# Performance work log

Hardware: AMD Instinct MI355X
Metric: run time of the kernel (lower is better)

Reference implementation:

```python
import jax, jax.numpy as jnp
import numpy as np

VOCAB = 32000
EMBED = 512
HIDDEN = 1024
ATT_L = 64
MAX_LEN = 32
BATCH = 64  # hardcoded in original get_start_states()


def setup_inputs() -> dict:
    key = jax.random.key(0)
    ks = jax.random.split(key, 12)
    s = 0.02
    return {
        "features": jax.random.normal(ks[0], (BATCH, ATT_L, HIDDEN), dtype=jnp.float32),
        "captions": jax.random.randint(ks[1], (BATCH, MAX_LEN), 0, VOCAB),
        "lengths": jnp.full((BATCH,), MAX_LEN - 1, dtype=jnp.int32),  # full lengths (sorted)
        "embed_table": jax.random.normal(ks[2], (VOCAB, EMBED), dtype=jnp.float32) * s,
        "W_ih": jax.random.normal(ks[3], (4 * HIDDEN, EMBED + HIDDEN), dtype=jnp.float32) * s,
        "W_hh": jax.random.normal(ks[4], (4 * HIDDEN, HIDDEN), dtype=jnp.float32) * s,
        "b_ih": jax.random.normal(ks[5], (4 * HIDDEN,), dtype=jnp.float32) * s,
        "b_hh": jax.random.normal(ks[6], (4 * HIDDEN,), dtype=jnp.float32) * s,
        "attn_W": jax.random.normal(ks[7], (ATT_L, EMBED + HIDDEN), dtype=jnp.float32) * s,
        "attn_b": jax.random.normal(ks[8], (ATT_L,), dtype=jnp.float32) * s,
        "lin_W": jax.random.normal(ks[9], (VOCAB, HIDDEN), dtype=jnp.float32) * s,
        "lin_b": jax.random.normal(ks[10], (VOCAB,), dtype=jnp.float32) * s,
    }


def reference(features, captions, lengths, embed_table, W_ih, W_hh, b_ih, b_hh,
              attn_W, attn_b, lin_W, lin_b):
    B = features.shape[0]
    T = captions.shape[1] - 1  # loop runs max_seq_length - 1 steps
    emb = embed_table[captions]              # (B, S, E)
    xs = jnp.transpose(emb[:, :T, :], (1, 0, 2))  # (T, B, E) time-major for scan

    h0 = jnp.zeros((B, HIDDEN), dtype=features.dtype)
    c0 = jnp.zeros((B, HIDDEN), dtype=features.dtype)

    def step(carry, x_t):
        h, c = carry
        # additive-attention branch (softmax over a singleton dim, as in original)
        att_cat = jnp.concatenate([x_t, h], axis=-1) @ attn_W.T + attn_b  # (B, L)
        att_w = jax.nn.softmax(jax.nn.relu(att_cat)[:, None, :], axis=1)  # (B, 1, L) -> all ones
        ctx = jnp.einsum('bol,blh->bh', att_w, features)                  # (B, H)
        # LSTM step (PyTorch gate order: i, f, g, o)
        lstm_in = jnp.concatenate([x_t, ctx], axis=-1)  # (B, E+H)
        gates = lstm_in @ W_ih.T + b_ih + h @ W_hh.T + b_hh
        i, f, g, o = jnp.split(gates, 4, axis=-1)
        c_new = jax.nn.sigmoid(f) * c + jax.nn.sigmoid(i) * jnp.tanh(g)
        h_new = jax.nn.sigmoid(o) * jnp.tanh(c_new)
        return (h_new, c_new), h_new

    _, hs = jax.lax.scan(step, (h0, c0), xs)  # (T, B, H)
    logits = hs @ lin_W.T + lin_b             # (T, B, V)
    # pack_padded_sequence with full lengths == time-major flatten
    return logits.reshape(T * B, -1)
```

## Files before the change

kernel.cpp:

```cpp
#include <hip/hip_runtime.h>
#include <hip/hip_bf16.h>
#include <stdint.h>

#define T_STEPS 31
#define B_ 64
#define E_ 512
#define H_ 1024
#define G4 4096
#define V_ 32000
#define MPAD 2048

typedef __bf16 bf16x8_t __attribute__((ext_vector_type(8)));
typedef float f32x4_t __attribute__((ext_vector_type(4)));
typedef unsigned short u16x8_t __attribute__((ext_vector_type(8)));
using bf16 = __hip_bfloat16;

typedef const __attribute__((address_space(1))) unsigned int gas_u32;
typedef __attribute__((address_space(3))) unsigned int las_u32;

__device__ __forceinline__ void async16(const bf16* g, bf16* l) {
    __builtin_amdgcn_global_load_lds((gas_u32*)(uintptr_t)g, (las_u32*)(uintptr_t)l, 16, 0, 0);
}

template<int BM, int BN>
__global__ __launch_bounds__(256)
void gemm_lds(const bf16* __restrict__ A, const bf16* __restrict__ BT,
              float* __restrict__ C, const float* __restrict__ bias,
              int M, int N, int K, int accumulate)
{
    constexpr int BK = 32;
    constexpr int WM = BM / 2, WN = BN / 2;
    constexpr int MI = WM / 16, NI = WN / 16;
    constexpr int AV = (BM * BK) / (8 * 256);
    constexpr int BV = (BN * BK) / (8 * 256);
    static_assert(AV >= 1 && BV >= 1, "tile too small for staging");

    __shared__ bf16 As[BM * BK];
    __shared__ bf16 Bs[BN * BK];

    const int tid = threadIdx.x;
    const int lane = tid & 63;
    const int w = tid >> 6;
    const int wr = w >> 1, wc = w & 1;
    const int quad = lane >> 4, l16 = lane & 15;
    const int m0 = blockIdx.x * BM;
    const int n0 = blockIdx.y * BN;

    f32x4_t acc[MI][NI];
#pragma unroll
    for (int i = 0; i < MI; i++)
#pragma unroll
        for (int j = 0; j < NI; j++) acc[i][j] = f32x4_t{0.f, 0.f, 0.f, 0.f};

    for (int kt = 0; kt < K; kt += BK) {
#pragma unroll
        for (int v = 0; v < AV; v++) {
            int idx = tid + v * 256;
            int row = idx >> 2, col = (idx & 3) << 3;
            async16(A + (size_t)(m0 + row) * K + kt + col, As + idx * 8);
        }
#pragma unroll
        for (int v = 0; v < BV; v++) {
            int idx = tid + v * 256;
            int row = idx >> 2, col = (idx & 3) << 3;
            async16(BT + (size_t)(n0 + row) * K + kt + col, Bs + idx * 8);
        }
        __syncthreads();

        bf16x8_t af[MI], bfr[NI];
#pragma unroll
        for (int i = 0; i < MI; i++)
            af[i] = __builtin_bit_cast(bf16x8_t,
                *reinterpret_cast<const u16x8_t*>(&As[(wr * WM + i * 16 + l16) * BK + quad * 8]));
#pragma unroll
        for (int j = 0; j < NI; j++)
            bfr[j] = __builtin_bit_cast(bf16x8_t,
                *reinterpret_cast<const u16x8_t*>(&Bs[(wc * WN + j * 16 + l16) * BK + quad * 8]));
#pragma unroll
        for (int i = 0; i < MI; i++)
#pragma unroll
            for (int j = 0; j < NI; j++)
                acc[i][j] = __builtin_amdgcn_mfma_f32_16x16x32_bf16(af[i], bfr[j], acc[i][j], 0, 0, 0);
        __syncthreads();
    }

#pragma unroll
    for (int i = 0; i < MI; i++) {
        int rbase = m0 + wr * WM + i * 16 + quad * 4;
#pragma unroll
        for (int j = 0; j < NI; j++) {
            int coln = n0 + wc * WN + j * 16 + l16;
            float badd = bias ? bias[coln] : 0.f;
#pragma unroll
            for (int r = 0; r < 4; r++) {
                int grow = rbase + r;
                if (grow < M) {
                    size_t ci = (size_t)grow * N + coln;
                    float val = acc[i][j][r] + badd;
                    if (accumulate) C[ci] += val; else C[ci] = val;
                }
            }
        }
    }
}

__global__ __launch_bounds__(256)
void step_fused(const bf16* __restrict__ h_in, const bf16* __restrict__ Whh,
                const float* __restrict__ pre_x, const float* __restrict__ ctxW,
                const float* __restrict__ bc, float* __restrict__ c,
                bf16* __restrict__ h_out, bf16* __restrict__ hs, int t)
{
    constexpr int BK = 32;
    constexpr int K = H_;
    __shared__ bf16 As[64 * BK];
    __shared__ bf16 Bs[64 * BK];
    __shared__ float gates[64 * 65];

    const int tid = threadIdx.x;
    const int lane = tid & 63;
    const int w = tid >> 6;
    const int wr = w >> 1, wc = w & 1;
    const int quad = lane >> 4, l16 = lane & 15;
    const int n0 = blockIdx.x * 64;

    f32x4_t acc[2][2];
#pragma unroll
    for (int i = 0; i < 2; i++)
#pragma unroll
        for (int j = 0; j < 2; j++) acc[i][j] = f32x4_t{0.f, 0.f, 0.f, 0.f};

    for (int kt = 0; kt < K; kt += BK) {
        {
            int row = tid >> 2, col = (tid & 3) << 3;
            async16(h_in + (size_t)row * K + kt + col, As + tid * 8);
            async16(Whh + (size_t)(n0 + row) * K + kt + col, Bs + tid * 8);
        }
        __syncthreads();
        bf16x8_t af[2], bfr[2];
#pragma unroll
        for (int i = 0; i < 2; i++)
            af[i] = __builtin_bit_cast(bf16x8_t,
                *reinterpret_cast<const u16x8_t*>(&As[(wr * 32 + i * 16 + l16) * BK + quad * 8]));
#pragma unroll
        for (int j = 0; j < 2; j++)
            bfr[j] = __builtin_bit_cast(bf16x8_t,
                *reinterpret_cast<const u16x8_t*>(&Bs[(wc * 32 + j * 16 + l16) * BK + quad * 8]));
#pragma unroll
        for (int i = 0; i < 2; i++)
#pragma unroll
            for (int j = 0; j < 2; j++)
                acc[i][j] = __builtin_amdgcn_mfma_f32_16x16x32_bf16(af[i], bfr[j], acc[i][j], 0, 0, 0);
        __syncthreads();
    }

#pragma unroll
    for (int i = 0; i < 2; i++) {
        int rbase = wr * 32 + i * 16 + quad * 4;
#pragma unroll
        for (int j = 0; j < 2; j++) {
            int col = wc * 32 + j * 16 + l16;
            int gcol = n0 + col;
            float badd = bc[gcol];
#pragma unroll
            for (int r = 0; r < 4; r++) {
                int b = rbase + r;
                gates[b * 65 + col] = acc[i][j][r] + badd
                    + pre_x[((size_t)t * B_ + b) * G4 + gcol]
                    + ctxW[(size_t)b * G4 + gcol];
            }
        }
    }
    __syncthreads();

#pragma unroll
    for (int v = 0; v < 4; v++) {
        int item = tid + v * 256;
        int b = item >> 4, jj = item & 15;
        float gi = gates[b * 65 + jj * 4 + 0];
        float gf = gates[b * 65 + jj * 4 + 1];
        float gg = gates[b * 65 + jj * 4 + 2];
        float go = gates[b * 65 + jj * 4 + 3];
        int j = (n0 >> 2) + jj;
        int idx = b * H_ + j;
        float si = 1.f / (1.f + expf(-gi));
        float sf = 1.f / (1.f + expf(-gf));
        float so = 1.f / (1.f + expf(-go));
        float cn = sf * c[idx] + si * tanhf(gg);
        float hn = so * tanhf(cn);
        c[idx] = cn;
        bf16 hb = __float2bfloat16(hn);
        h_out[idx] = hb;
        hs[((size_t)t * B_ + b) * H_ + j] = hb;
    }
}


__global__ void ctx_kernel(const float* __restrict__ features, bf16* __restrict__ hi, bf16* __restrict__ lo)
{
    int b = blockIdx.x;
    for (int j = threadIdx.x; j < H_; j += 256) {
        float s = 0.f;
        const float* f = features + (size_t)b * 64 * H_ + j;
#pragma unroll
        for (int l = 0; l < 64; l++) s += f[(size_t)l * H_];
        bf16 h = __float2bfloat16(s);
        hi[b * H_ + j] = h;
        lo[b * H_ + j] = __float2bfloat16(s - __bfloat162float(h));
    }
}

__global__ void bias_kernel(const float* __restrict__ bi, const float* __restrict__ bh, float* __restrict__ bc)
{
    int g = blockIdx.x * 256 + threadIdx.x;
    if (g < G4) bc[(g & (H_ - 1)) * 4 + (g >> 10)] = bi[g] + bh[g];
}

__global__ void gather_embed(const int* __restrict__ captions, const float* __restrict__ table,
                             bf16* __restrict__ xs)
{
    int idx = blockIdx.x * 256 + threadIdx.x;
    int tb = idx >> 9, e = idx & (E_ - 1);
    float v = 0.f;
    if (tb < T_STEPS * B_) {
        int t = tb >> 6, b = tb & 63;
        int tok = captions[b * 32 + t];
        v = table[(size_t)tok * E_ + e];
    }
    xs[idx] = __float2bfloat16(v);
}

__global__ void cvt_bf16(const float* __restrict__ src, bf16* __restrict__ hi, bf16* __restrict__ lo,
                         int rows, int cols, int stride, int off, int perm)
{
    long i4 = (long)blockIdx.x * 256 + threadIdx.x;
    long total = (long)rows * cols / 4;
    if (i4 >= total) return;
    long e = i4 * 4;
    int r = (int)(e / cols);
    int ci = (int)(e % cols);
    int ro = perm ? ((r & (H_ - 1)) * 4 + (r >> 10)) : r;
    f32x4_t v = *reinterpret_cast<const f32x4_t*>(src + (size_t)r * stride + off + ci);
    size_t ob = (size_t)ro * cols + ci;
#pragma unroll
    for (int q = 0; q < 4; q++) {
        bf16 h = __float2bfloat16(v[q]);
        hi[ob + q] = h;
        if (lo) lo[ob + q] = __float2bfloat16(v[q] - __bfloat162float(h));
    }
}

__global__ void zero_f32(float* __restrict__ p, int n)
{
    int i = blockIdx.x * 256 + threadIdx.x;
    if (i < n) p[i] = 0.f;
}
__global__ void zero_bf16(bf16* __restrict__ p, int n)
{
    int i = blockIdx.x * 256 + threadIdx.x;
    if (i < n) p[i] = __float2bfloat16(0.f);
}

extern "C" void kernel_launch(void* const* d_in, const int* in_sizes, int n_in,
                              void* d_out, int out_size, void* d_ws, size_t ws_size,
                              hipStream_t stream)
{
    (void)in_sizes; (void)n_in; (void)out_size; (void)ws_size;
    const float* features = (const float*)d_in[0];
    const int*   captions = (const int*)d_in[1];
    const float* embed    = (const float*)d_in[3];
    const float* W_ih     = (const float*)d_in[4];
    const float* W_hh     = (const float*)d_in[5];
    const float* b_ih     = (const float*)d_in[6];
    const float* b_hh     = (const float*)d_in[7];
    const float* lin_W    = (const float*)d_in[10];
    const float* lin_b    = (const float*)d_in[11];
    float* out = (float*)d_out;

    char* wp = (char*)d_ws;
    auto alloc = [&](size_t bytes) -> void* {
        void* p = (void*)wp;
        wp += (bytes + 255) & ~(size_t)255;
        return p;
    };
    bf16*  ctx_hi = (bf16*)alloc((size_t)B_ * H_ * 2);
    bf16*  ctx_lo = (bf16*)alloc((size_t)B_ * H_ * 2);
    float* bc     = (float*)alloc((size_t)G4 * 4);
    bf16*  xs     = (bf16*)alloc((size_t)MPAD * E_ * 2);
    bf16*  Wx     = (bf16*)alloc((size_t)G4 * E_ * 2);
    bf16*  Wc_hi  = (bf16*)alloc((size_t)G4 * H_ * 2);
    bf16*  Wc_lo  = (bf16*)alloc((size_t)G4 * H_ * 2);
    bf16*  Whh    = (bf16*)alloc((size_t)G4 * H_ * 2);
    bf16*  WlinB  = (bf16*)alloc((size_t)V_ * H_ * 2);
    float* pre_x  = (float*)alloc((size_t)T_STEPS * B_ * G4 * 4);
    float* ctxW   = (float*)alloc((size_t)B_ * G4 * 4);
    float* cbuf   = (float*)alloc((size_t)B_ * H_ * 4);
    bf16*  h_bf   = (bf16*)alloc((size_t)B_ * H_ * 2);
    bf16*  hs     = (bf16*)alloc((size_t)MPAD * H_ * 2);

    bias_kernel<<<16, 256, 0, stream>>>(b_ih, b_hh, bc);
    ctx_kernel<<<B_, 256, 0, stream>>>(features, ctx_hi, ctx_lo);
    gather_embed<<<MPAD * E_ / 256, 256, 0, stream>>>(captions, embed, xs);
    cvt_bf16<<<G4 * E_ / 4 / 256, 256, 0, stream>>>(W_ih, Wx, nullptr, G4, E_, E_ + H_, 0, 1);
    cvt_bf16<<<G4 * H_ / 4 / 256, 256, 0, stream>>>(W_ih, Wc_hi, Wc_lo, G4, H_, E_ + H_, E_, 1);
    cvt_bf16<<<G4 * H_ / 4 / 256, 256, 0, stream>>>(W_hh, Whh, nullptr, G4, H_, H_, 0, 1);
    cvt_bf16<<<V_ * (H_ / 4) / 256, 256, 0, stream>>>(lin_W, WlinB, nullptr, V_, H_, H_, 0, 0);
    zero_f32<<<B_ * H_ / 256, 256, 0, stream>>>(cbuf, B_ * H_);
    zero_bf16<<<B_ * H_ / 256, 256, 0, stream>>>(h_bf, B_ * H_);
    zero_bf16<<<(MPAD - T_STEPS * B_) * H_ / 256, 256, 0, stream>>>(
        hs + (size_t)T_STEPS * B_ * H_, (MPAD - T_STEPS * B_) * H_);

    gemm_lds<64, 64><<<dim3(1, G4 / 64), 256, 0, stream>>>(ctx_hi, Wc_hi, ctxW, nullptr, B_, G4, H_, 0);
    gemm_lds<64, 64><<<dim3(1, G4 / 64), 256, 0, stream>>>(ctx_lo, Wc_hi, ctxW, nullptr, B_, G4, H_, 1);
    gemm_lds<64, 64><<<dim3(1, G4 / 64), 256, 0, stream>>>(ctx_hi, Wc_lo, ctxW, nullptr, B_, G4, H_, 1);

    gemm_lds<128, 128><<<dim3(MPAD / 128, G4 / 128), 256, 0, stream>>>(
        xs, Wx, pre_x, nullptr, T_STEPS * B_, G4, E_, 0);

    for (int t = 0; t < T_STEPS; t++)
        step_fused<<<G4 / 64, 256, 0, stream>>>(h_bf, Whh, pre_x, ctxW, bc, cbuf, h_bf, hs, t);

    gemm_lds<128, 128><<<dim3(MPAD / 128, V_ / 128), 256, 0, stream>>>(
        hs, WlinB, out, lin_b, T_STEPS * B_, V_, H_, 0);
}
```

Baseline: 1.220 ms.

## Replace per-step LSTM launches with persistent recurrence kernel and XCD-aware GEMM tiling

The 31 per-timestep launches become one persistent kernel of 64 workgroups. Each workgroup keeps its 64-row slice of W_hh resident in swizzled LDS (128 KB) and the cell state in registers, and uses an atomic grid barrier between steps. This removes per-step launch overhead and the repeated reloading of W_hh from global memory. Separately, the GEMMs now use a 1D grid remapped so that neighbouring tiles land on the same XCD for better L2 reuse. The risks are that the spin barrier can deadlock if all 64 blocks are not co-resident, and that h is read directly from global memory on each step.

```diff
diff --git a/kernel.cpp b/kernel.cpp
--- a/kernel.cpp
+++ b/kernel.cpp
@@ -9,6 +9,7 @@
 #define G4 4096
 #define V_ 32000
 #define MPAD 2048
+#define NREC 64
 
 typedef __bf16 bf16x8_t __attribute__((ext_vector_type(8)));
 typedef float f32x4_t __attribute__((ext_vector_type(4)));
@@ -26,7 +27,7 @@
 __global__ __launch_bounds__(256)
 void gemm_lds(const bf16* __restrict__ A, const bf16* __restrict__ BT,
               float* __restrict__ C, const float* __restrict__ bias,
-              int M, int N, int K, int accumulate)
+              int M, int N, int K, int accumulate, int mblocks)
 {
     constexpr int BK = 32;
     constexpr int WM = BM / 2, WN = BN / 2;
@@ -43,8 +44,14 @@
     const int w = tid >> 6;
     const int wr = w >> 1, wc = w & 1;
     const int quad = lane >> 4, l16 = lane & 15;
-    const int m0 = blockIdx.x * BM;
-    const int n0 = blockIdx.y * BN;
+
+    const int nwg = gridDim.x;
+    const int bid = blockIdx.x;
+    const int q = nwg >> 3, r = nwg & 7;
+    const int xcd = bid & 7, o = bid >> 3;
+    const int wgid = (xcd < r ? xcd * (q + 1) : r * (q + 1) + (xcd - r) * q) + o;
+    const int m0 = (wgid % mblocks) * BM;
+    const int n0 = (wgid / mblocks) * BN;
 
     f32x4_t acc[MI][NI];
 #pragma unroll
@@ -104,16 +111,25 @@
     }
 }
 
+__device__ __forceinline__ void grid_barrier(int* bar, int target) {
+    __syncthreads();
+    if (threadIdx.x == 0) {
+        __threadfence();
+        atomicAdd(bar, 1);
+        while (__hip_atomic_load(bar, __ATOMIC_ACQUIRE, __HIP_MEMORY_SCOPE_AGENT) < target)
+            __builtin_amdgcn_s_sleep(2);
+        __threadfence();
+    }
+    __syncthreads();
+}
+
 __global__ __launch_bounds__(256)
-void step_fused(const bf16* __restrict__ h_in, const bf16* __restrict__ Whh,
-                const float* __restrict__ pre_x, const float* __restrict__ ctxW,
-                const float* __restrict__ bc, float* __restrict__ c,
-                bf16* __restrict__ h_out, bf16* __restrict__ hs, int t)
-{
-    constexpr int BK = 32;
-    constexpr int K = H_;
-    __shared__ bf16 As[64 * BK];
-    __shared__ bf16 Bs[64 * BK];
+void recurrence(const bf16* __restrict__ h0, bf16* __restrict__ hs,
+                const bf16* __restrict__ Whh, const float* __restrict__ pre_x,
+                const float* __restrict__ ctxW, const float* __restrict__ bc,
+                int* __restrict__ bar)
+{
+    __shared__ bf16 Wl[64 * H_];
     __shared__ float gates[64 * 65];
 
     const int tid = threadIdx.x;
@@ -123,74 +139,87 @@
     const int quad = lane >> 4, l16 = lane & 15;
     const int n0 = blockIdx.x * 64;
 
-    f32x4_t acc[2][2];
-#pragma unroll
-    for (int i = 0; i < 2; i++)
-#pragma unroll
-        for (int j = 0; j < 2; j++) acc[i][j] = f32x4_t{0.f, 0.f, 0.f, 0.f};
-
-    for (int kt = 0; kt < K; kt += BK) {
-        {
-            int row = tid >> 2, col = (tid & 3) << 3;
-            async16(h_in + (size_t)row * K + kt + col, As + tid * 8);
-            async16(Whh + (size_t)(n0 + row) * K + kt + col, Bs + tid * 8);
+#pragma unroll 4
+    for (int ck = tid; ck < 64 * 128; ck += 256) {
+        int row = ck >> 7, c16 = ck & 127;
+        u16x8_t v = *reinterpret_cast<const u16x8_t*>(Whh + (size_t)(n0 + row) * H_ + (c16 << 3));
+        int byte = (row << 11) + (((c16 << 4)) ^ ((row & 7) << 4));
+        *reinterpret_cast<u16x8_t*>(reinterpret_cast<char*>(Wl) + byte) = v;
+    }
+
+    float creg[4] = {0.f, 0.f, 0.f, 0.f};
+    __syncthreads();
+
+    const int arow = wr * 32 + l16;
+    const int r0 = wc * 32 + l16;
+    const int xr = (r0 & 7) << 4;
+    const char* wl0 = reinterpret_cast<const char*>(Wl) + (r0 << 11);
+    const char* wl1 = reinterpret_cast<const char*>(Wl) + ((r0 + 16) << 11);
+
+    int target = NREC;
+    for (int t = 0; t < T_STEPS; t++) {
+        const bf16* hp = t ? hs + (size_t)(t - 1) * B_ * H_ : h0;
+        const bf16* ha0 = hp + (size_t)arow * H_ + quad * 8;
+        const bf16* ha1 = ha0 + 16 * H_;
+
+        f32x4_t acc[2][2];
+#pragma unroll
+        for (int i = 0; i < 2; i++)
+#pragma unroll
+            for (int j = 0; j < 2; j++) acc[i][j] = f32x4_t{0.f, 0.f, 0.f, 0.f};
+
+#pragma unroll 4
+        for (int kt = 0; kt < H_; kt += 32) {
+            int off = ((kt << 1) + (quad << 4)) ^ xr;
+            bf16x8_t a0 = __builtin_bit_cast(bf16x8_t, *reinterpret_cast<const u16x8_t*>(ha0 + kt));
+            bf16x8_t a1 = __builtin_bit_cast(bf16x8_t, *reinterpret_cast<const u16x8_t*>(ha1 + kt));
+            bf16x8_t b0 = __builtin_bit_cast(bf16x8_t, *reinterpret_cast<const u16x8_t*>(wl0 + off));
+            bf16x8_t b1 = __builtin_bit_cast(bf16x8_t, *reinterpret_cast<const u16x8_t*>(wl1 + off));
+            acc[0][0] = __builtin_amdgcn_mfma_f32_16x16x32_bf16(a0, b0, acc[0][0], 0, 0, 0);
+            acc[0][1] = __builtin_amdgcn_mfma_f32_16x16x32_bf16(a0, b1, acc[0][1], 0, 0, 0);
+            acc[1][0] = __builtin_amdgcn_mfma_f32_16x16x32_bf16(a1, b0, acc[1][0], 0, 0, 0);
+            acc[1][1] = __builtin_amdgcn_mfma_f32_16x16x32_bf16(a1, b1, acc[1][1], 0, 0, 0);
+        }
+
+#pragma unroll
+        for (int i = 0; i < 2; i++) {
+            int rbase = wr * 32 + i * 16 + quad * 4;
+#pragma unroll
+            for (int j = 0; j < 2; j++) {
+                int col = wc * 32 + j * 16 + l16;
+                int gcol = n0 + col;
+                float badd = bc[gcol];
+#pragma unroll
+                for (int r = 0; r < 4; r++) {
+                    int b = rbase + r;
+                    gates[b * 65 + col] = acc[i][j][r] + badd
+                        + pre_x[((size_t)t * B_ + b) * G4 + gcol]
+                        + ctxW[(size_t)b * G4 + gcol];
+                }
+            }
         }
         __syncthreads();
-        bf16x8_t af[2], bfr[2];
-#pragma unroll
-        for (int i = 0; i < 2; i++)
-            af[i] = __builtin_bit_cast(bf16x8_t,
-                *reinterpret_cast<const u16x8_t*>(&As[(wr * 32 + i * 16 + l16) * BK + quad * 8]));
-#pragma unroll
-        for (int j = 0; j < 2; j++)
-            bfr[j] = __builtin_bit_cast(bf16x8_t,
-                *reinterpret_cast<const u16x8_t*>(&Bs[(wc * 32 + j * 16 + l16) * BK + quad * 8]));
-#pragma unroll
-        for (int i = 0; i < 2; i++)
-#pragma unroll
-            for (int j = 0; j < 2; j++)
-                acc[i][j] = __builtin_amdgcn_mfma_f32_16x16x32_bf16(af[i], bfr[j], acc[i][j], 0, 0, 0);
-        __syncthreads();
-    }
-
-#pragma unroll
-    for (int i = 0; i < 2; i++) {
-        int rbase = wr * 32 + i * 16 + quad * 4;
-#pragma unroll
-        for (int j = 0; j < 2; j++) {
-            int col = wc * 32 + j * 16 + l16;
-            int gcol = n0 + col;
-            float badd = bc[gcol];
-#pragma unroll
-            for (int r = 0; r < 4; r++) {
-                int b = rbase + r;
-                gates[b * 65 + col] = acc[i][j][r] + badd
-                    + pre_x[((size_t)t * B_ + b) * G4 + gcol]
-                    + ctxW[(size_t)b * G4 + gcol];
-            }
-        }
-    }
-    __syncthreads();
-
-#pragma unroll
-    for (int v = 0; v < 4; v++) {
-        int item = tid + v * 256;
-        int b = item >> 4, jj = item & 15;
-        float gi = gates[b * 65 + jj * 4 + 0];
-        float gf = gates[b * 65 + jj * 4 + 1];
-        float gg = gates[b * 65 + jj * 4 + 2];
-        float go = gates[b * 65 + jj * 4 + 3];
-        int j = (n0 >> 2) + jj;
-        int idx = b * H_ + j;
-        float si = 1.f / (1.f + expf(-gi));
-        float sf = 1.f / (1.f + expf(-gf));
-        float so = 1.f / (1.f + expf(-go));
-        float cn = sf * c[idx] + si * tanhf(gg);
-        float hn = so * tanhf(cn);
-        c[idx] = cn;
-        bf16 hb = __float2bfloat16(hn);
-        h_out[idx] = hb;
-        hs[((size_t)t * B_ + b) * H_ + j] = hb;
+
+#pragma unroll
+        for (int v = 0; v < 4; v++) {
+            int item = tid + v * 256;
+            int b = item >> 4, jj = item & 15;
+            float gi = gates[b * 65 + jj * 4 + 0];
+            float gf = gates[b * 65 + jj * 4 + 1];
+            float gg = gates[b * 65 + jj * 4 + 2];
+            float go = gates[b * 65 + jj * 4 + 3];
+            int j = (n0 >> 2) + jj;
+            float si = 1.f / (1.f + expf(-gi));
+            float sf = 1.f / (1.f + expf(-gf));
+            float so = 1.f / (1.f + expf(-go));
+            float cn = sf * creg[v] + si * tanhf(gg);
+            float hn = so * tanhf(cn);
+            creg[v] = cn;
+            hs[((size_t)t * B_ + b) * H_ + j] = __float2bfloat16(hn);
+        }
+
+        grid_barrier(bar, target);
+        target += NREC;
     }
 }
 
@@ -293,9 +322,9 @@
     bf16*  WlinB  = (bf16*)alloc((size_t)V_ * H_ * 2);
     float* pre_x  = (float*)alloc((size_t)T_STEPS * B_ * G4 * 4);
     float* ctxW   = (float*)alloc((size_t)B_ * G4 * 4);
-    float* cbuf   = (float*)alloc((size_t)B_ * H_ * 4);
-    bf16*  h_bf   = (bf16*)alloc((size_t)B_ * H_ * 2);
+    bf16*  h0     = (bf16*)alloc((size_t)B_ * H_ * 2);
     bf16*  hs     = (bf16*)alloc((size_t)MPAD * H_ * 2);
+    int*   bar    = (int*)alloc(256);
 
     bias_kernel<<<16, 256, 0, stream>>>(b_ih, b_hh, bc);
     ctx_kernel<<<B_, 256, 0, stream>>>(features, ctx_hi, ctx_lo);
@@ -304,21 +333,20 @@
     cvt_bf16<<<G4 * H_ / 4 / 256, 256, 0, stream>>>(W_ih, Wc_hi, Wc_lo, G4, H_, E_ + H_, E_, 1);
     cvt_bf16<<<G4 * H_ / 4 / 256, 256, 0, stream>>>(W_hh, Whh, nullptr, G4, H_, H_, 0, 1);
     cvt_bf16<<<V_ * (H_ / 4) / 256, 256, 0, stream>>>(lin_W, WlinB, nullptr, V_, H_, H_, 0, 0);
-    zero_f32<<<B_ * H_ / 256, 256, 0, stream>>>(cbuf, B_ * H_);
-    zero_bf16<<<B_ * H_ / 256, 256, 0, stream>>>(h_bf, B_ * H_);
+    zero_bf16<<<B_ * H_ / 256, 256, 0, stream>>>(h0, B_ * H_);
     zero_bf16<<<(MPAD - T_STEPS * B_) * H_ / 256, 256, 0, stream>>>(
         hs + (size_t)T_STEPS * B_ * H_, (MPAD - T_STEPS * B_) * H_);
-
-    gemm_lds<64, 64><<<dim3(1, G4 / 64), 256, 0, stream>>>(ctx_hi, Wc_hi, ctxW, nullptr, B_, G4, H_, 0);
-    gemm_lds<64, 64><<<dim3(1, G4 / 64), 256, 0, stream>>>(ctx_lo, Wc_hi, ctxW, nullptr, B_, G4, H_, 1);
-    gemm_lds<64, 64><<<dim3(1, G4 / 64), 256, 0, stream>>>(ctx_hi, Wc_lo, ctxW, nullptr, B_, G4, H_, 1);
-
-    gemm_lds<128, 128><<<dim3(MPAD / 128, G4 / 128), 256, 0, stream>>>(
-        xs, Wx, pre_x, nullptr, T_STEPS * B_, G4, E_, 0);
-
-    for (int t = 0; t < T_STEPS; t++)
-        step_fused<<<G4 / 64, 256, 0, stream>>>(h_bf, Whh, pre_x, ctxW, bc, cbuf, h_bf, hs, t);
-
-    gemm_lds<128, 128><<<dim3(MPAD / 128, V_ / 128), 256, 0, stream>>>(
-        hs, WlinB, out, lin_b, T_STEPS * B_, V_, H_, 0);
-}
+    zero_f32<<<1, 256, 0, stream>>>((float*)bar, 1);
+
+    gemm_lds<64, 64><<<G4 / 64, 256, 0, stream>>>(ctx_hi, Wc_hi, ctxW, nullptr, B_, G4, H_, 0, 1);
+    gemm_lds<64, 64><<<G4 / 64, 256, 0, stream>>>(ctx_lo, Wc_hi, ctxW, nullptr, B_, G4, H_, 1, 1);
+    gemm_lds<64, 64><<<G4 / 64, 256, 0, stream>>>(ctx_hi, Wc_lo, ctxW, nullptr, B_, G4, H_, 1, 1);
+
+    gemm_lds<128, 128><<<(MPAD / 128) * (G4 / 128), 256, 0, stream>>>(
+        xs, Wx, pre_x, nullptr, T_STEPS * B_, G4, E_, 0, MPAD / 128);
+
+    recurrence<<<NREC, 256, 0, stream>>>(h0, hs, Whh, pre_x, ctxW, bc, bar);
+
+    gemm_lds<128, 128><<<(MPAD / 128) * (V_ / 128), 256, 0, stream>>>(
+        hs, WlinB, out, lin_b, T_STEPS * B_, V_, H_, 0, MPAD / 128);
+}
```

Result: slower. 1.291 ms (+5.8%).
